# Optimization experiments

Hardware: AMD Instinct MI355X
Metric: run time of the kernel (lower is better)

## Reference

```python
import jax, jax.numpy as jnp
import numpy as np

NEG_SLOPE = 0.2
EPS = 1e-16


def gat_layer(x, src, dst, W, a_src, a_dst, b, concat):
    """PyG GATConv (add_self_loops already applied to src/dst)."""
    N = x.shape[0]
    H, C = a_src.shape
    h = (x @ W).reshape(N, H, C)                      # [N,H,C]
    al_s = jnp.einsum('nhc,hc->nh', h, a_src)          # [N,H]
    al_d = jnp.einsum('nhc,hc->nh', h, a_dst)          # [N,H]
    e = jax.nn.leaky_relu(al_s[src] + al_d[dst], NEG_SLOPE)  # [E,H]
    m = jax.ops.segment_max(e, dst, num_segments=N)    # per-dst max
    ex = jnp.exp(e - m[dst])
    s = jax.ops.segment_sum(ex, dst, num_segments=N)
    alpha = ex / (s[dst] + EPS)                        # [E,H]
    out = jax.ops.segment_sum(alpha[:, :, None] * h[src], dst, num_segments=N)  # [N,H,C]
    out = out.reshape(N, H * C) if concat else out.mean(axis=1)
    return out + b


def setup_inputs() -> dict:
    key = jax.random.key(0)
    ks = jax.random.split(key, 10)
    N, E, IN, HID, OUT, HEADS = 50000, 800000, 128, 128, 64, 4
    return {
        'x': jax.random.normal(ks[0], (N, IN), jnp.float32),
        'edge_index': jax.random.randint(ks[1], (2, E), 0, N, jnp.int32),
        'W1': jax.random.normal(ks[2], (IN, HID), jnp.float32) * 0.1,
        'a1_src': jax.random.normal(ks[3], (HEADS, HID // HEADS), jnp.float32) * 0.1,
        'a1_dst': jax.random.normal(ks[4], (HEADS, HID // HEADS), jnp.float32) * 0.1,
        'b1': jax.random.normal(ks[5], (HID,), jnp.float32) * 0.1,
        'W2': jax.random.normal(ks[6], (HID, OUT), jnp.float32) * 0.1,
        'a2_src': jax.random.normal(ks[7], (1, OUT), jnp.float32) * 0.1,
        'a2_dst': jax.random.normal(ks[8], (1, OUT), jnp.float32) * 0.1,
        'b2': jax.random.normal(ks[9], (OUT,), jnp.float32) * 0.1,
    }


def reference(x, edge_index, W1, a1_src, a1_dst, b1, W2, a2_src, a2_dst, b2):
    N = x.shape[0]
    loops = jnp.arange(N, dtype=edge_index.dtype)
    src = jnp.concatenate([edge_index[0], loops])
    dst = jnp.concatenate([edge_index[1], loops])
    # layer 1 (concat heads) -> ELU -> dropout(identity in eval)
    h = jax.nn.elu(gat_layer(x, src, dst, W1, a1_src, a1_dst, b1, concat=True))
    # layer 2 (heads=1, concat=False -> mean)
    return gat_layer(h, src, dst, W2, a2_src, a2_dst, b2, concat=False)
```

## Files before the change

### kernel.cpp

```cpp
#include <hip/hip_runtime.h>
#include <hip/hip_bf16.h>
#include <cstdint>
#include <cstddef>

#define IN_F 128
#define HID 128
#define NH1 4
#define OUTF 64
#define NBMAX 512
#define CH 2048
#define NBFILL 256

typedef __attribute__((ext_vector_type(8))) short short8;
typedef __attribute__((ext_vector_type(4))) float f32x4;

__device__ __forceinline__ float lrelu(float v) { return v > 0.f ? v : 0.2f * v; }
__device__ __forceinline__ float eluf(float v) { return v > 0.f ? v : (__expf(v) - 1.f); }
__device__ __forceinline__ unsigned f2bf(float f) {
  unsigned u = __float_as_uint(f);
  return (u + 0x7fffu + ((u >> 16) & 1u)) >> 16;
}
__device__ __forceinline__ float bflo(unsigned hv) { return __uint_as_float(hv << 16); }
__device__ __forceinline__ float bfhi(unsigned hv) { return __uint_as_float(hv & 0xffff0000u); }

__global__ __launch_bounds__(256) void k_pb(
    const float* __restrict__ x, const float* __restrict__ W1, const float* __restrict__ W2,
    const int* __restrict__ dst, int E,
    unsigned short* __restrict__ xb, unsigned short* __restrict__ wt,
    unsigned short* __restrict__ wt2, int* __restrict__ gbcnt, int nx4) {
  __shared__ int bcnt[NBMAX];
  if (blockIdx.x < 512) {
    const int t = threadIdx.x;
    bcnt[t] = 0; bcnt[t + 256] = 0;
    __syncthreads();
    for (int e = blockIdx.x * 256 + t; e < E; e += 512 * 256)
      atomicAdd(&bcnt[dst[e] >> 7], 1);
    __syncthreads();
    for (int b = t; b < NBMAX; b += 256)
      if (bcnt[b]) atomicAdd(&gbcnt[b], bcnt[b]);
    return;
  }
  const int t = (blockIdx.x - 512) * 256 + threadIdx.x;
  if (t < nx4) {
    const float4 v = ((const float4*)x)[t];
    uint2 u;
    u.x = f2bf(v.x) | (f2bf(v.y) << 16);
    u.y = f2bf(v.z) | (f2bf(v.w) << 16);
    ((uint2*)xb)[t] = u;
  }
  if (t < IN_F * HID) {
    const int k = t >> 7, c = t & 127;
    const int chunk = k >> 3;
    const int csw = (chunk & 8) | ((chunk ^ (c & 7)) & 7);
    wt[c * 128 + csw * 8 + (k & 7)] = (unsigned short)f2bf(W1[t]);
  }
  if (t < HID * OUTF) {
    const int k = t >> 6, c = t & 63;
    const int chunk = k >> 3;
    const int csw = (chunk & 8) | ((chunk ^ (c & 7)) & 7);
    wt2[c * 128 + csw * 8 + (k & 7)] = (unsigned short)f2bf(W2[t]);
  }
}

__global__ __launch_bounds__(512) void k_bscan(const int* __restrict__ gbcnt,
                                               int* __restrict__ sbase,
                                               int* __restrict__ gcursor,
                                               int* __restrict__ csrbase,
                                               int NB, int N) {
  __shared__ int tmp[NBMAX];
  const int t = threadIdx.x;
  const int g = (t < NB) ? gbcnt[t] : 0;
  const int nsz = (t < NB) ? min(128, N - t * 128) : 0;
  tmp[t] = g;
  __syncthreads();
  #pragma unroll
  for (int off = 1; off < NBMAX; off <<= 1) {
    const int v = (t >= off) ? tmp[t - off] : 0;
    __syncthreads();
    tmp[t] += v;
    __syncthreads();
  }
  const int sb = tmp[t] - g;
  if (t < NB) { sbase[t] = sb; gcursor[t] = sb; }
  __syncthreads();
  tmp[t] = g + nsz;
  __syncthreads();
  #pragma unroll
  for (int off = 1; off < NBMAX; off <<= 1) {
    const int v = (t >= off) ? tmp[t - off] : 0;
    __syncthreads();
    tmp[t] += v;
    __syncthreads();
  }
  if (t < NB) csrbase[t] = tmp[t] - (g + nsz);
}

__global__ __launch_bounds__(256) void k_g1bf(
    const unsigned short* __restrict__ xb, const unsigned short* __restrict__ wt,
    const float* __restrict__ a_s, const float* __restrict__ a_d,
    unsigned* __restrict__ h16, float* __restrict__ als, float* __restrict__ ald, int N,
    const int* __restrict__ src, const int* __restrict__ dst, int E,
    int* __restrict__ gcursor, unsigned* __restrict__ stage, int NG1) {
  __shared__ __align__(16) unsigned char smem[32768];
  if ((int)blockIdx.x >= NG1) {
    int* bcnt = (int*)smem;
    int* bofs = bcnt + NBMAX;
    int* lcur = bofs + NBMAX;
    int* gofs = lcur + NBMAX;
    unsigned* obuf = (unsigned*)(smem + 8192);
    unsigned short* bid = (unsigned short*)(smem + 16384);
    const int t = threadIdx.x;
    const int b = blockIdx.x - NG1;
    for (int base_e = b * CH; base_e < E; base_e += NBFILL * CH) {
      const int cnt = min(CH, E - base_e);
      __syncthreads();
      bcnt[t] = 0; bcnt[t + 256] = 0;
      __syncthreads();
      for (int i = t; i < cnt; i += 256)
        atomicAdd(&bcnt[dst[base_e + i] >> 7], 1);
      __syncthreads();
      bofs[t] = bcnt[t]; bofs[t + 256] = bcnt[t + 256];
      __syncthreads();
      #pragma unroll
      for (int off = 1; off < NBMAX; off <<= 1) {
        const int v0 = (t >= off) ? bofs[t - off] : 0;
        const int v1 = (t + 256 >= off) ? bofs[t + 256 - off] : 0;
        __syncthreads();
        bofs[t] += v0; bofs[t + 256] += v1;
        __syncthreads();
      }
      {
        const int e0 = bofs[t] - bcnt[t], e1 = bofs[t + 256] - bcnt[t + 256];
        __syncthreads();
        bofs[t] = e0;        bofs[t + 256] = e1;
        lcur[t] = e0;        lcur[t + 256] = e1;
      }
      __syncthreads();
      for (int i = t; i < cnt; i += 256) {
        const int d = dst[base_e + i];
        const int bb = d >> 7;
        const int pos = atomicAdd(&lcur[bb], 1);
        obuf[pos] = ((unsigned)(d & 127) << 25) | (unsigned)src[base_e + i];
        bid[pos] = (unsigned short)bb;
      }
      __syncthreads();
      for (int bb = t; bb < NBMAX; bb += 256)
        if (bcnt[bb] > 0) gofs[bb] = atomicAdd(&gcursor[bb], bcnt[bb]);
      __syncthreads();
      for (int i = t; i < cnt; i += 256) {
        const int bb = bid[i];
        stage[gofs[bb] + (i - bofs[bb])] = obuf[i];
      }
    }
    return;
  }
  unsigned short* Wl = (unsigned short*)smem;
  const int wave = threadIdx.x >> 6, lane = threadIdx.x & 63;
  for (int i = threadIdx.x * 8; i < IN_F * HID; i += 256 * 8)
    *(short8*)(Wl + i) = *(const short8*)(wt + i);
  __syncthreads();
  const int li = lane & 15, g = lane >> 4;
  const int r0w = blockIdx.x * 64 + wave * 16;
  if (r0w >= N) return;
  float asp[8], adp[8];
  #pragma unroll
  for (int nt = 0; nt < 8; ++nt) { asp[nt] = a_s[16 * nt + li]; adp[nt] = a_d[16 * nt + li]; }
  f32x4 acc[8];
  #pragma unroll
  for (int nt = 0; nt < 8; ++nt) acc[nt] = (f32x4){0.f, 0.f, 0.f, 0.f};
  const int arow = min(r0w + li, N - 1);
  const unsigned short* xrow = xb + (size_t)arow * IN_F;
  #pragma unroll
  for (int s = 0; s < 4; ++s) {
    const short8 a = *(const short8*)(xrow + 32 * s + g * 8);
    const int chunk = 4 * s + g;
    const int csw = (chunk & 8) | ((chunk ^ (li & 7)) & 7);
    const unsigned short* bbase = Wl + li * 128 + csw * 8;
    #pragma unroll
    for (int nt = 0; nt < 8; ++nt) {
      const short8 bfr = *(const short8*)(bbase + nt * 2048);
      acc[nt] = __builtin_amdgcn_mfma_f32_16x16x32_bf16(a, bfr, acc[nt], 0, 0, 0);
    }
  }
  #pragma unroll
  for (int r = 0; r < 4; ++r) {
    const int row = r0w + g * 4 + r;
    if (row < N) {
      #pragma unroll
      for (int nt = 0; nt < 4; ++nt) {
        const unsigned u = f2bf(acc[nt][r]) | (f2bf(acc[nt + 4][r]) << 16);
        h16[(size_t)row * 64 + 16 * nt + li] = u;
      }
    }
  }
  #pragma unroll
  for (int r = 0; r < 4; ++r) {
    const int row = r0w + g * 4 + r;
    #pragma unroll
    for (int hh = 0; hh < 4; ++hh) {
      float ps = acc[2 * hh][r] * asp[2 * hh] + acc[2 * hh + 1][r] * asp[2 * hh + 1];
      float pd = acc[2 * hh][r] * adp[2 * hh] + acc[2 * hh + 1][r] * adp[2 * hh + 1];
      #pragma unroll
      for (int mk = 1; mk <= 8; mk <<= 1) {
        ps += __shfl_xor(ps, mk, 16);
        pd += __shfl_xor(pd, mk, 16);
      }
      if (li == 0 && row < N) {
        als[row * NH1 + hh] = ps;
        ald[row * NH1 + hh] = pd;
      }
    }
  }
}

__global__ __launch_bounds__(256) void k_build(const unsigned* __restrict__ stage,
                                               const int* __restrict__ sbase,
                                               const int* __restrict__ gbcnt,
                                               const int* __restrict__ csrbase,
                                               int* __restrict__ rowptr,
                                               int* __restrict__ counts,
                                               int* __restrict__ csr, int N) {
  __shared__ int lc[128], lofs[128], lcur[128];
  const int b = blockIdx.x;
  const int t = threadIdx.x;
  const int n0 = b << 7;
  const int nn = min(128, N - n0);
  if (t < 128) lc[t] = (t < nn) ? 1 : 0;
  __syncthreads();
  const int s0 = sbase[b], ecnt = gbcnt[b];
  for (int i = t; i < ecnt; i += 256)
    atomicAdd(&lc[stage[s0 + i] >> 25], 1);
  __syncthreads();
  if (t < 128) lofs[t] = lc[t];
  __syncthreads();
  #pragma unroll
  for (int off = 1; off < 128; off <<= 1) {
    const int v = (t >= off && t < 128) ? lofs[t - off] : 0;
    __syncthreads();
    if (t < 128) lofs[t] += v;
    __syncthreads();
  }
  const int base = csrbase[b];
  if (t < nn) {
    const int ex = lofs[t] - lc[t];
    const int r = base + ex;
    rowptr[n0 + t] = r;
    counts[n0 + t] = lc[t];
    csr[r] = n0 + t;
    lcur[t] = ex + 1;
  }
  __syncthreads();
  for (int i = t; i < ecnt; i += 256) {
    const unsigned e = stage[s0 + i];
    const int d = e >> 25;
    const int pos = atomicAdd(&lcur[d], 1);
    csr[base + pos] = (int)(e & 0x1FFFFFFu);
  }
}

__global__ __launch_bounds__(256) void k_gemm2(
    const unsigned short* __restrict__ hb, const unsigned short* __restrict__ wt2,
    const float* __restrict__ a_s, const float* __restrict__ a_d,
    unsigned* __restrict__ h16, float* __restrict__ als, float* __restrict__ ald, int N) {
  __shared__ unsigned short Wl[OUTF * HID];
  const int wave = threadIdx.x >> 6, lane = threadIdx.x & 63;
  for (int i = threadIdx.x * 8; i < OUTF * HID; i += 256 * 8)
    *(short8*)(Wl + i) = *(const short8*)(wt2 + i);
  __syncthreads();
  const int li = lane & 15, g = lane >> 4;
  const int r0w = blockIdx.x * 64 + wave * 16;
  if (r0w >= N) return;
  float asp[4], adp[4];
  #pragma unroll
  for (int nt = 0; nt < 4; ++nt) { asp[nt] = a_s[16 * nt + li]; adp[nt] = a_d[16 * nt + li]; }
  f32x4 acc[4];
  #pragma unroll
  for (int nt = 0; nt < 4; ++nt) acc[nt] = (f32x4){0.f, 0.f, 0.f, 0.f};
  const int arow = min(r0w + li, N - 1);
  const unsigned short* xrow = hb + (size_t)arow * HID;
  #pragma unroll
  for (int s = 0; s < 4; ++s) {
    const short8 a = *(const short8*)(xrow + 32 * s + g * 8);
    const int chunk = 4 * s + g;
    const int csw = (chunk & 8) | ((chunk ^ (li & 7)) & 7);
    const unsigned short* bbase = Wl + li * 128 + csw * 8;
    #pragma unroll
    for (int nt = 0; nt < 4; ++nt) {
      const short8 bfr = *(const short8*)(bbase + nt * 2048);
      acc[nt] = __builtin_amdgcn_mfma_f32_16x16x32_bf16(a, bfr, acc[nt], 0, 0, 0);
    }
  }
  #pragma unroll
  for (int r = 0; r < 4; ++r) {
    const int row = r0w + g * 4 + r;
    #pragma unroll
    for (int nt = 0; nt < 4; ++nt) {
      const float v = acc[nt][r];
      const float vn = __shfl_xor(v, 1, 64);
      if (!(li & 1) && row < N)
        h16[(size_t)row * 32 + 8 * nt + (li >> 1)] = f2bf(v) | (f2bf(vn) << 16);
    }
  }
  #pragma unroll
  for (int r = 0; r < 4; ++r) {
    const int row = r0w + g * 4 + r;
    float ps = 0.f, pd = 0.f;
    #pragma unroll
    for (int nt = 0; nt < 4; ++nt) { ps += acc[nt][r] * asp[nt]; pd += acc[nt][r] * adp[nt]; }
    #pragma unroll
    for (int mk = 1; mk <= 8; mk <<= 1) {
      ps += __shfl_xor(ps, mk, 16);
      pd += __shfl_xor(pd, mk, 16);
    }
    if (li == 0 && row < N) { als[row] = ps; ald[row] = pd; }
  }
}

__global__ __launch_bounds__(256) void k_aggr1(
    const int* __restrict__ rowptr, const int* __restrict__ counts,
    const int* __restrict__ csr,
    const float* __restrict__ als, const float* __restrict__ ald,
    const unsigned* __restrict__ h16, const float* __restrict__ b,
    unsigned short* __restrict__ outb, int N) {
  const int lane = threadIdx.x & 63;
  const int d = blockIdx.x * 4 + (threadIdx.x >> 6);
  if (d >= N) return;
  const int row0 = rowptr[d], deg = counts[d];
  const int headE = lane & 3;
  const float aldE = ald[d * NH1 + headE];
  const int hx = lane >> 5, hy = 2 + hx;
  const float bx = b[lane], by = b[lane + 64];
  float psum = 0.f, ax = 0.f, ay = 0.f;
  int i = 0;
  for (; i + 8 <= deg; i += 8) {
    const int sl = (lane < 8) ? csr[row0 + i + lane] : 0;
    const int se = __shfl(sl, lane >> 2, 64);
    const float pv = __expf(lrelu(als[se * NH1 + headE] + aldE));
    if (lane < 32) psum += pv;
    #pragma unroll
    for (int j = 0; j < 8; ++j) {
      const int s = __builtin_amdgcn_readfirstlane(__shfl(sl, j, 64));
      const unsigned hv = h16[(size_t)s * 64 + lane];
      const float px = __shfl(pv, 4 * j + hx, 64);
      const float py = __shfl(pv, 4 * j + hy, 64);
      ax += px * bflo(hv);
      ay += py * bfhi(hv);
    }
  }
  if (i < deg) {
    const int rem = deg - i;
    const int sl = (lane < 8) ? csr[row0 + i + min(lane, rem - 1)] : 0;
    const int se = __shfl(sl, lane >> 2, 64);
    float pv = __expf(lrelu(als[se * NH1 + headE] + aldE));
    if ((lane >> 2) >= rem) pv = 0.f;
    if (lane < 32) psum += pv;
    #pragma unroll
    for (int j = 0; j < 8; ++j) {
      const int s = __builtin_amdgcn_readfirstlane(__shfl(sl, j, 64));
      const unsigned hv = h16[(size_t)s * 64 + lane];
      const float px = __shfl(pv, 4 * j + hx, 64);
      const float py = __shfl(pv, 4 * j + hy, 64);
      ax += px * bflo(hv);
      ay += py * bfhi(hv);
    }
  }
  #pragma unroll
  for (int mk = 4; mk <= 16; mk <<= 1) psum += __shfl_xor(psum, mk, 32);
  const float sumx = __shfl(psum, hx, 64);
  const float sumy = __shfl(psum, hy, 64);
  outb[(size_t)d * HID + lane]      = (unsigned short)f2bf(eluf(ax / (sumx + 1e-16f) + bx));
  outb[(size_t)d * HID + 64 + lane] = (unsigned short)f2bf(eluf(ay / (sumy + 1e-16f) + by));
}

__global__ __launch_bounds__(256) void k_aggr2(
    const int* __restrict__ rowptr, const int* __restrict__ counts,
    const int* __restrict__ csr,
    const float* __restrict__ als, const float* __restrict__ ald,
    const unsigned* __restrict__ h16, const float* __restrict__ b,
    float* __restrict__ out, int N) {
  const int lane = threadIdx.x & 63;
  const int d = blockIdx.x * 4 + (threadIdx.x >> 6);
  if (d >= N) return;
  const int row0 = rowptr[d], deg = counts[d];
  const float aldd = ald[d];
  const int eo = lane >> 5;
  const int c = lane & 31;
  float psum = 0.f, a0 = 0.f, a1 = 0.f;
  int i = 0;
  for (; i + 16 <= deg; i += 16) {
    const int sl = (lane < 16) ? csr[row0 + i + lane] : 0;
    const float pv = __expf(lrelu(als[sl] + aldd));
    if (lane < 16) psum += pv;
    #pragma unroll
    for (int q = 0; q < 8; ++q) {
      const int s = __shfl(sl, 2 * q + eo, 64);
      const float p = __shfl(pv, 2 * q + eo, 64);
      const unsigned hv = h16[(size_t)s * (OUTF / 2) + c];
      a0 += p * bflo(hv);
      a1 += p * bfhi(hv);
    }
  }
  if (i < deg) {
    const int rem = deg - i;
    const int sl = (lane < 16) ? csr[row0 + i + min(lane, rem - 1)] : 0;
    float pv = __expf(lrelu(als[sl] + aldd));
    if (lane >= rem) pv = 0.f;
    if (lane < 16) psum += pv;
    #pragma unroll
    for (int q = 0; q < 8; ++q) {
      const int s = __shfl(sl, 2 * q + eo, 64);
      const float p = __shfl(pv, 2 * q + eo, 64);
      const unsigned hv = h16[(size_t)s * (OUTF / 2) + c];
      a0 += p * bflo(hv);
      a1 += p * bfhi(hv);
    }
  }
  #pragma unroll
  for (int mk = 1; mk <= 8; mk <<= 1) psum += __shfl_xor(psum, mk, 16);
  a0 += __shfl_xor(a0, 32, 64);
  a1 += __shfl_xor(a1, 32, 64);
  if (lane < 32) {
    const float r = 1.f / (__shfl(psum, 0, 64) + 1e-16f);
    float2 o;
    o.x = a0 * r + b[2 * c];
    o.y = a1 * r + b[2 * c + 1];
    *(float2*)(out + (size_t)d * OUTF + 2 * c) = o;
  }
}

extern "C" void kernel_launch(void* const* d_in, const int* in_sizes, int n_in,
                              void* d_out, int out_size, void* d_ws, size_t ws_size,
                              hipStream_t stream) {
  const float* x   = (const float*)d_in[0];
  const int*   ei  = (const int*)d_in[1];
  const float* W1  = (const float*)d_in[2];
  const float* a1s = (const float*)d_in[3];
  const float* a1d = (const float*)d_in[4];
  const float* b1  = (const float*)d_in[5];
  const float* W2  = (const float*)d_in[6];
  const float* a2s = (const float*)d_in[7];
  const float* a2d = (const float*)d_in[8];
  const float* b2  = (const float*)d_in[9];
  float* out = (float*)d_out;

  const int N = in_sizes[0] / IN_F;
  const int E = in_sizes[1] / 2;
  const int ET = E + N;
  const int* srcI = ei;
  const int* dstI = ei + E;
  const int NB = (N + 127) >> 7;
  const int NG1 = (N + 63) / 64;

  int* rowptr  = (int*)d_ws;
  int* counts  = rowptr + N;
  int* csr     = counts + N;
  unsigned* stage = (unsigned*)(csr + ET);
  int* gbcnt   = (int*)(stage + E);
  int* sbase   = gbcnt + NBMAX;
  int* csrbase = sbase + NBMAX;
  int* gcursor = csrbase + NBMAX;
  size_t int_end = (size_t)(2 * N + ET + E + 4 * NBMAX);
  int_end = (int_end + 3) & ~(size_t)3;
  float* h1f   = (float*)d_ws + int_end;
  unsigned* h16 = (unsigned*)h1f;
  unsigned short* xb = (unsigned short*)(h1f + (size_t)N * 64);
  unsigned short* out1b = (unsigned short*)(h1f + (size_t)N * HID);
  float* alf   = h1f + (size_t)N * HID + (size_t)N * 64;
  float* al1s_ = alf;
  float* al1d_ = al1s_ + (size_t)N * NH1;
  float* al2s_ = al1d_ + (size_t)N * NH1;
  float* al2d_ = al2s_ + N;
  unsigned short* wt  = (unsigned short*)(al2d_ + N);
  unsigned short* wt2 = wt + IN_F * HID;

  const int nx4 = N * IN_F / 4;
  const int nprep = (nx4 + 255) / 256;

  hipMemsetAsync(gbcnt, 0, NBMAX * sizeof(int), stream);
  k_pb<<<512 + nprep, 256, 0, stream>>>(x, W1, W2, dstI, E, xb, wt, wt2, gbcnt, nx4);
  k_bscan<<<1, 512, 0, stream>>>(gbcnt, sbase, gcursor, csrbase, NB, N);
  k_g1bf<<<NG1 + NBFILL, 256, 0, stream>>>(xb, wt, a1s, a1d, h16, al1s_, al1d_, N,
                                           srcI, dstI, E, gcursor, stage, NG1);
  k_build<<<NB, 256, 0, stream>>>(stage, sbase, gbcnt, csrbase, rowptr, counts, csr, N);

  k_aggr1<<<(N + 3) / 4, 256, 0, stream>>>(rowptr, counts, csr, al1s_, al1d_, h16, b1, out1b, N);

  k_gemm2<<<(N + 63) / 64, 256, 0, stream>>>(out1b, wt2, a2s, a2d, h16, al2s_, al2d_, N);
  k_aggr2<<<(N + 3) / 4, 256, 0, stream>>>(rowptr, counts, csr, al2s_, al2d_, h16, b2, out, N);
}
```

Before: 142.8 us.

## Split GAT aggregation kernels into two feature-half passes with contiguous h layout

Layer-1 h16 storage is reordered so adjacent column pairs are packed contiguously, letting each aggregation pass read one contiguous half of a row. Both aggregation kernels are templated on a feature half and launched twice, each wavefront processing more edges per iteration over a narrower slice. The intent is to shrink the per-pass gather working set for better cache locality and to raise edge-level parallelism. In exchange, the CSR indices and attention logits are read and the exponentials recomputed twice, and there are extra kernel launches.

```diff
diff --git a/kernel.cpp b/kernel.cpp
--- a/kernel.cpp
+++ b/kernel.cpp
@@ -185,12 +185,12 @@
   #pragma unroll
   for (int r = 0; r < 4; ++r) {
     const int row = r0w + g * 4 + r;
-    if (row < N) {
-      #pragma unroll
-      for (int nt = 0; nt < 4; ++nt) {
-        const unsigned u = f2bf(acc[nt][r]) | (f2bf(acc[nt + 4][r]) << 16);
-        h16[(size_t)row * 64 + 16 * nt + li] = u;
-      }
+    #pragma unroll
+    for (int nt = 0; nt < 8; ++nt) {
+      const float v = acc[nt][r];
+      const float vn = __shfl_xor(v, 1, 64);
+      if (!(li & 1) && row < N)
+        h16[(size_t)row * 64 + 8 * nt + (li >> 1)] = f2bf(v) | (f2bf(vn) << 16);
     }
   }
   #pragma unroll
@@ -316,6 +316,7 @@
   }
 }
 
+template <int HALF>
 __global__ __launch_bounds__(256) void k_aggr1(
     const int* __restrict__ rowptr, const int* __restrict__ counts,
     const int* __restrict__ csr,
@@ -326,52 +327,58 @@
   const int d = blockIdx.x * 4 + (threadIdx.x >> 6);
   if (d >= N) return;
   const int row0 = rowptr[d], deg = counts[d];
-  const int headE = lane & 3;
-  const float aldE = ald[d * NH1 + headE];
-  const int hx = lane >> 5, hy = 2 + hx;
-  const float bx = b[lane], by = b[lane + 64];
-  float psum = 0.f, ax = 0.f, ay = 0.f;
+  const int c = lane & 31;
+  const int eo = lane >> 5;
+  const int headP = 2 * HALF + (lane & 1);
+  const float aldP = ald[d * NH1 + headP];
+  const float b0 = b[64 * HALF + 2 * c], b1 = b[64 * HALF + 2 * c + 1];
+  float psum = 0.f, a0 = 0.f, a1 = 0.f;
   int i = 0;
-  for (; i + 8 <= deg; i += 8) {
-    const int sl = (lane < 8) ? csr[row0 + i + lane] : 0;
-    const int se = __shfl(sl, lane >> 2, 64);
-    const float pv = __expf(lrelu(als[se * NH1 + headE] + aldE));
+  for (; i + 16 <= deg; i += 16) {
+    const int sl = (lane < 16) ? csr[row0 + i + lane] : 0;
+    const int se = __shfl(sl, lane >> 1, 64);
+    const float pv = __expf(lrelu(als[se * NH1 + headP] + aldP));
     if (lane < 32) psum += pv;
     #pragma unroll
-    for (int j = 0; j < 8; ++j) {
-      const int s = __builtin_amdgcn_readfirstlane(__shfl(sl, j, 64));
-      const unsigned hv = h16[(size_t)s * 64 + lane];
-      const float px = __shfl(pv, 4 * j + hx, 64);
-      const float py = __shfl(pv, 4 * j + hy, 64);
-      ax += px * bflo(hv);
-      ay += py * bfhi(hv);
+    for (int q = 0; q < 8; ++q) {
+      const int j = 2 * q + eo;
+      const int s = __shfl(sl, j, 64);
+      const float p = __shfl(pv, 2 * j + (c >> 4), 64);
+      const unsigned hv = h16[(size_t)s * 64 + 32 * HALF + c];
+      a0 += p * bflo(hv);
+      a1 += p * bfhi(hv);
     }
   }
   if (i < deg) {
     const int rem = deg - i;
-    const int sl = (lane < 8) ? csr[row0 + i + min(lane, rem - 1)] : 0;
-    const int se = __shfl(sl, lane >> 2, 64);
-    float pv = __expf(lrelu(als[se * NH1 + headE] + aldE));
-    if ((lane >> 2) >= rem) pv = 0.f;
+    const int sl = (lane < 16) ? csr[row0 + i + min(lane, rem - 1)] : 0;
+    const int se = __shfl(sl, lane >> 1, 64);
+    float pv = __expf(lrelu(als[se * NH1 + headP] + aldP));
+    if ((lane >> 1) >= rem) pv = 0.f;
     if (lane < 32) psum += pv;
     #pragma unroll
-    for (int j = 0; j < 8; ++j) {
-      const int s = __builtin_amdgcn_readfirstlane(__shfl(sl, j, 64));
-      const unsigned hv = h16[(size_t)s * 64 + lane];
-      const float px = __shfl(pv, 4 * j + hx, 64);
-      const float py = __shfl(pv, 4 * j + hy, 64);
-      ax += px * bflo(hv);
-      ay += py * bfhi(hv);
-    }
-  }
-  #pragma unroll
-  for (int mk = 4; mk <= 16; mk <<= 1) psum += __shfl_xor(psum, mk, 32);
-  const float sumx = __shfl(psum, hx, 64);
-  const float sumy = __shfl(psum, hy, 64);
-  outb[(size_t)d * HID + lane]      = (unsigned short)f2bf(eluf(ax / (sumx + 1e-16f) + bx));
-  outb[(size_t)d * HID + 64 + lane] = (unsigned short)f2bf(eluf(ay / (sumy + 1e-16f) + by));
-}
-
+    for (int q = 0; q < 8; ++q) {
+      const int j = 2 * q + eo;
+      const int s = __shfl(sl, j, 64);
+      const float p = __shfl(pv, 2 * j + (c >> 4), 64);
+      const unsigned hv = h16[(size_t)s * 64 + 32 * HALF + c];
+      a0 += p * bflo(hv);
+      a1 += p * bfhi(hv);
+    }
+  }
+  #pragma unroll
+  for (int mk = 2; mk <= 16; mk <<= 1) psum += __shfl_xor(psum, mk, 32);
+  const float sum = __shfl(psum, c >> 4, 64);
+  a0 += __shfl_xor(a0, 32, 64);
+  a1 += __shfl_xor(a1, 32, 64);
+  if (lane < 32) {
+    const float r = 1.f / (sum + 1e-16f);
+    const unsigned u = f2bf(eluf(a0 * r + b0)) | (f2bf(eluf(a1 * r + b1)) << 16);
+    ((unsigned*)(outb + (size_t)d * HID + 64 * HALF))[c] = u;
+  }
+}
+
+template <int HALF>
 __global__ __launch_bounds__(256) void k_aggr2(
     const int* __restrict__ rowptr, const int* __restrict__ counts,
     const int* __restrict__ csr,
@@ -383,48 +390,53 @@
   if (d >= N) return;
   const int row0 = rowptr[d], deg = counts[d];
   const float aldd = ald[d];
-  const int eo = lane >> 5;
-  const int c = lane & 31;
+  const int g4 = lane >> 4;
+  const int c = lane & 15;
   float psum = 0.f, a0 = 0.f, a1 = 0.f;
   int i = 0;
-  for (; i + 16 <= deg; i += 16) {
-    const int sl = (lane < 16) ? csr[row0 + i + lane] : 0;
+  for (; i + 32 <= deg; i += 32) {
+    const int sl = (lane < 32) ? csr[row0 + i + lane] : 0;
     const float pv = __expf(lrelu(als[sl] + aldd));
-    if (lane < 16) psum += pv;
+    if (lane < 32) psum += pv;
     #pragma unroll
     for (int q = 0; q < 8; ++q) {
-      const int s = __shfl(sl, 2 * q + eo, 64);
-      const float p = __shfl(pv, 2 * q + eo, 64);
-      const unsigned hv = h16[(size_t)s * (OUTF / 2) + c];
+      const int j = 4 * q + g4;
+      const int s = __shfl(sl, j, 64);
+      const float p = __shfl(pv, j, 64);
+      const unsigned hv = h16[(size_t)s * 32 + 16 * HALF + c];
       a0 += p * bflo(hv);
       a1 += p * bfhi(hv);
     }
   }
   if (i < deg) {
     const int rem = deg - i;
-    const int sl = (lane < 16) ? csr[row0 + i + min(lane, rem - 1)] : 0;
+    const int sl = (lane < 32) ? csr[row0 + i + min(lane, rem - 1)] : 0;
     float pv = __expf(lrelu(als[sl] + aldd));
     if (lane >= rem) pv = 0.f;
-    if (lane < 16) psum += pv;
+    if (lane < 32) psum += pv;
     #pragma unroll
     for (int q = 0; q < 8; ++q) {
-      const int s = __shfl(sl, 2 * q + eo, 64);
-      const float p = __shfl(pv, 2 * q + eo, 64);
-      const unsigned hv = h16[(size_t)s * (OUTF / 2) + c];
+      const int j = 4 * q + g4;
+      const int s = __shfl(sl, j, 64);
+      const float p = __shfl(pv, j, 64);
+      const unsigned hv = h16[(size_t)s * 32 + 16 * HALF + c];
       a0 += p * bflo(hv);
       a1 += p * bfhi(hv);
     }
   }
   #pragma unroll
-  for (int mk = 1; mk <= 8; mk <<= 1) psum += __shfl_xor(psum, mk, 16);
+  for (int mk = 1; mk <= 16; mk <<= 1) psum += __shfl_xor(psum, mk, 32);
+  const float sum = __shfl(psum, 0, 64);
+  a0 += __shfl_xor(a0, 16, 64);
+  a1 += __shfl_xor(a1, 16, 64);
   a0 += __shfl_xor(a0, 32, 64);
   a1 += __shfl_xor(a1, 32, 64);
-  if (lane < 32) {
-    const float r = 1.f / (__shfl(psum, 0, 64) + 1e-16f);
+  if (lane < 16) {
+    const float r = 1.f / (sum + 1e-16f);
     float2 o;
-    o.x = a0 * r + b[2 * c];
-    o.y = a1 * r + b[2 * c + 1];
-    *(float2*)(out + (size_t)d * OUTF + 2 * c) = o;
+    o.x = a0 * r + b[32 * HALF + 2 * c];
+    o.y = a1 * r + b[32 * HALF + 2 * c + 1];
+    ((float2*)(out + (size_t)d * OUTF + 32 * HALF))[c] = o;
   }
 }
 
@@ -483,8 +495,11 @@
                                            srcI, dstI, E, gcursor, stage, NG1);
   k_build<<<NB, 256, 0, stream>>>(stage, sbase, gbcnt, csrbase, rowptr, counts, csr, N);
 
-  k_aggr1<<<(N + 3) / 4, 256, 0, stream>>>(rowptr, counts, csr, al1s_, al1d_, h16, b1, out1b, N);
+  const int ga = (N + 3) / 4;
+  k_aggr1<0><<<ga, 256, 0, stream>>>(rowptr, counts, csr, al1s_, al1d_, h16, b1, out1b, N);
+  k_aggr1<1><<<ga, 256, 0, stream>>>(rowptr, counts, csr, al1s_, al1d_, h16, b1, out1b, N);
 
   k_gemm2<<<(N + 63) / 64, 256, 0, stream>>>(out1b, wt2, a2s, a2d, h16, al2s_, al2d_, N);
-  k_aggr2<<<(N + 3) / 4, 256, 0, stream>>>(rowptr, counts, csr, al2s_, al2d_, h16, b2, out, N);
-}
+  k_aggr2<0><<<ga, 256, 0, stream>>>(rowptr, counts, csr, al2s_, al2d_, h16, b2, out, N);
+  k_aggr2<1><<<ga, 256, 0, stream>>>(rowptr, counts, csr, al2s_, al2d_, h16, b2, out, N);
+}
```

Measured after the change: 178.8 us. 1.25x slower.
